# Performance work log

Measured on AMD Instinct MI355X. Metric: run time of the kernel, lower is better.

## Reference

```python
import jax, jax.numpy as jnp
import numpy as np

NUM_HEADS = 8
NUM_GROUPS = 32  # min(32, channels=256)
EPS = 1e-5


def group_norm(x, w, b):
    # x: [B, C, L]
    B, C, L = x.shape
    xg = x.reshape(B, NUM_GROUPS, C // NUM_GROUPS, L)
    mu = xg.mean(axis=(2, 3), keepdims=True)
    var = xg.var(axis=(2, 3), keepdims=True)
    xn = ((xg - mu) * jax.lax.rsqrt(var + EPS)).reshape(B, C, L)
    return xn * w[None, :, None] + b[None, :, None]


def setup_inputs() -> dict:
    key = jax.random.key(0)
    ks = jax.random.split(key, 5)
    B, C, L = 4, 256, 2048
    x = jax.random.normal(ks[0], (B, C, L), dtype=jnp.float32)
    gn_w = jnp.ones((C,), dtype=jnp.float32)
    gn_b = jnp.zeros((C,), dtype=jnp.float32)
    qkv_w = jax.random.normal(ks[1], (3 * C, C), dtype=jnp.float32) * (C ** -0.5)
    qkv_b = jax.random.normal(ks[2], (3 * C,), dtype=jnp.float32) * 0.02
    out_w = jax.random.normal(ks[3], (C, C), dtype=jnp.float32) * (C ** -0.5)
    out_b = jax.random.normal(ks[4], (C,), dtype=jnp.float32) * 0.02
    return {"x": x, "gn_w": gn_w, "gn_b": gn_b, "qkv_w": qkv_w,
            "qkv_b": qkv_b, "out_w": out_w, "out_b": out_b}


def reference(x, gn_w, gn_b, qkv_w, qkv_b, out_w, out_b):
    B, C, L = x.shape
    H = NUM_HEADS
    D = C // H
    h = group_norm(x, gn_w, gn_b)
    # 1x1 conv == channel matmul: [B,3C,L]
    qkv = jnp.einsum('oc,bcl->bol', qkv_w, h) + qkv_b[None, :, None]
    qkv = qkv.reshape(B, 3, H, D, L)
    q, k, v = qkv[:, 0], qkv[:, 1], qkv[:, 2]  # each [B,H,D,L]
    scale = D ** -0.5
    attn = jnp.einsum('bhdn,bhdm->bhnm', q * scale, k)  # [B,H,L,L]
    attn = jax.nn.softmax(attn, axis=-1)
    h = jnp.einsum('bhnm,bhdm->bhdn', attn, v).reshape(B, C, L)
    out = jnp.einsum('oc,bcl->bol', out_w, h) + out_b[None, :, None]
    return x + out
```

## Files before the change

### kernel.cpp

```cpp
#include <hip/hip_runtime.h>
#include <math.h>

using f32x4  = __attribute__((ext_vector_type(4))) float;
using bf16x8 = __attribute__((ext_vector_type(8))) short;

constexpr int kB = 4, kC = 256, kL = 2048, kH = 8;
constexpr float kQScale = 0.25505402264f;

__device__ __forceinline__ unsigned short f2bf(float f) {
    unsigned u = __builtin_bit_cast(unsigned, f);
    u += 0x7fffu + ((u >> 16) & 1u);
    return (unsigned short)(u >> 16);
}
__device__ __forceinline__ unsigned cvt_pk(float lo, float hi) {
    unsigned r;
    asm("v_cvt_pk_bf16_f32 %0, %1, %2" : "=v"(r) : "v"(lo), "v"(hi));
    return r;
}
__device__ __forceinline__ f32x4 mfma16(bf16x8 a, bf16x8 b, f32x4 c) {
    return __builtin_amdgcn_mfma_f32_16x16x32_bf16(a, b, c, 0, 0, 0);
}
__device__ __forceinline__ bf16x8 bc8(unsigned a, unsigned b, unsigned c, unsigned d) {
    return __builtin_bit_cast(bf16x8, make_uint4(a, b, c, d));
}
__device__ __forceinline__ void glds16(const unsigned short* g, unsigned short* l) {
    __builtin_amdgcn_global_load_lds(
        (const __attribute__((address_space(1))) unsigned int*)g,
        (__attribute__((address_space(3))) unsigned int*)l, 16, 0, 0);
}

__global__ __launch_bounds__(256) void gncvt_kernel(const float* __restrict__ x,
                                                    const float* __restrict__ gw,
                                                    const float* __restrict__ gb,
                                                    unsigned short* __restrict__ hT,
                                                    const float* __restrict__ qkvw,
                                                    const float* __restrict__ outw,
                                                    unsigned short* __restrict__ wq,
                                                    unsigned short* __restrict__ wo) {
    if (blockIdx.x >= 128) {
        int i = (blockIdx.x - 128) * 256 + threadIdx.x;
        const float* s; unsigned short* d; int j;
        if (i < 49152) { s = qkvw; d = wq; j = i; }
        else           { s = outw; d = wo; j = i - 49152; }
        float4 v = ((const float4*)s)[j];
        ((uint2*)d)[j] = make_uint2(cvt_pk(v.x, v.y), cvt_pk(v.z, v.w));
        return;
    }
    int b = blockIdx.x >> 5, g = blockIdx.x & 31;
    int t = threadIdx.x;
    const float* xp = x + ((size_t)b * kC + g * 8) * kL + 8 * t;

    float v[8][8];
    float s = 0.f, ss = 0.f;
#pragma unroll
    for (int c = 0; c < 8; ++c) {
        float4 a  = *(const float4*)(xp + (size_t)c * kL);
        float4 a2 = *(const float4*)(xp + (size_t)c * kL + 4);
        v[c][0]=a.x; v[c][1]=a.y; v[c][2]=a.z; v[c][3]=a.w;
        v[c][4]=a2.x; v[c][5]=a2.y; v[c][6]=a2.z; v[c][7]=a2.w;
        s  += (a.x+a.y)+(a.z+a.w)+(a2.x+a2.y)+(a2.z+a2.w);
        ss += a.x*a.x+a.y*a.y+a.z*a.z+a.w*a.w+a2.x*a2.x+a2.y*a2.y+a2.z*a2.z+a2.w*a2.w;
    }
#pragma unroll
    for (int off = 32; off; off >>= 1) {
        s  += __shfl_down(s, off);
        ss += __shfl_down(ss, off);
    }
    __shared__ float red[8];
    int wv = t >> 6;
    if ((t & 63) == 0) { red[wv] = s; red[4 + wv] = ss; }
    __syncthreads();
    s  = red[0] + red[1] + red[2] + red[3];
    ss = red[4] + red[5] + red[6] + red[7];
    float mean = s * (1.f / 16384.f);
    float var  = ss * (1.f / 16384.f) - mean * mean;
    float rstd = rsqrtf(var + 1e-5f);

    float wc[8], bc[8];
#pragma unroll
    for (int c = 0; c < 8; ++c) { wc[c] = gw[g*8+c] * rstd; bc[c] = gb[g*8+c]; }

    unsigned short* hp = hT + ((size_t)b * kL + 8 * t) * kC + g * 8;
#pragma unroll
    for (int j = 0; j < 8; ++j) {
        unsigned pk[4];
#pragma unroll
        for (int c2 = 0; c2 < 4; ++c2) {
            pk[c2] = cvt_pk((v[2*c2  ][j] - mean) * wc[2*c2  ] + bc[2*c2  ],
                            (v[2*c2+1][j] - mean) * wc[2*c2+1] + bc[2*c2+1]);
        }
        *(uint4*)(hp + (size_t)j * kC) = make_uint4(pk[0], pk[1], pk[2], pk[3]);
    }
}

__device__ __forceinline__ void store_qk(unsigned short* __restrict__ base, size_t bh,
                                         int n, int d0, f32x4 acc,
                                         const float* bias4, float scale) {
    float v0 = (acc[0] + bias4[0]) * scale, v1 = (acc[1] + bias4[1]) * scale;
    float v2 = (acc[2] + bias4[2]) * scale, v3 = (acc[3] + bias4[3]) * scale;
    *(uint2*)(base + (bh * kL + n) * 32 + d0) = make_uint2(cvt_pk(v0, v1), cvt_pk(v2, v3));
}

__global__ __launch_bounds__(256) void qkv_gemm(const unsigned short* __restrict__ Wb,
                                                const unsigned short* __restrict__ hT,
                                                const float* __restrict__ qkvb,
                                                unsigned short* __restrict__ qT,
                                                unsigned short* __restrict__ kT,
                                                unsigned short* __restrict__ vbuf) {
    __shared__ alignas(16) unsigned short Hlds[2][8][512];
    int t = threadIdx.x, wv = t >> 6, ll = t & 15, lg = (t >> 4) & 3;
    int lane = t & 63;
    int n0 = blockIdx.x * 128, o0 = blockIdx.y * 64, b = blockIdx.z;
    int obase = o0 + wv * 16;
    const unsigned short* hb = hT + (size_t)b * kL * kC;

    bf16x8 wf[8];
#pragma unroll
    for (int k = 0; k < 8; ++k)
        wf[k] = *(const bf16x8*)(Wb + (size_t)(obase + ll) * 256 + 32 * k + 8 * lg);
    float bias[4];
#pragma unroll
    for (int r = 0; r < 4; ++r) bias[r] = qkvb[obase + 4 * lg + r];
    int mode = (obase < 256) ? 0 : (obase < 512 ? 1 : 2);
    int d0 = (obase & 31) + 4 * lg;

    const unsigned short* hsrc0 = hb + (size_t)(n0 + 16 * (2 * wv)     + ll) * 256 + 8 * lg;
    const unsigned short* hsrc1 = hb + (size_t)(n0 + 16 * (2 * wv + 1) + ll) * 256 + 8 * lg;

    glds16(hsrc0,      &Hlds[0][2 * wv][0]);
    glds16(hsrc1,      &Hlds[0][2 * wv + 1][0]);
    glds16(hsrc0 + 32, &Hlds[1][2 * wv][0]);
    glds16(hsrc1 + 32, &Hlds[1][2 * wv + 1][0]);
    asm volatile("s_waitcnt vmcnt(2)" ::: "memory");
    __builtin_amdgcn_sched_barrier(0);
    __builtin_amdgcn_s_barrier();

    f32x4 acc[8] = {};
    int cur = 0;
    for (int c = 0; c < 8; ++c) {
        bf16x8 hf[8];
#pragma unroll
        for (int nj = 0; nj < 8; ++nj)
            hf[nj] = *(const bf16x8*)&Hlds[cur][nj][lane * 8];
        asm volatile("s_waitcnt lgkmcnt(0)" ::: "memory");
        __builtin_amdgcn_sched_barrier(0);
        __builtin_amdgcn_s_barrier();

        int kn = ((c + 2) & 7) * 32;
        glds16(hsrc0 + kn, &Hlds[cur][2 * wv][0]);
        glds16(hsrc1 + kn, &Hlds[cur][2 * wv + 1][0]);

        __builtin_amdgcn_s_setprio(1);
#pragma unroll
        for (int nj = 0; nj < 8; ++nj)
            acc[nj] = mfma16(wf[c], hf[nj], acc[nj]);
        __builtin_amdgcn_s_setprio(0);

        asm volatile("s_waitcnt vmcnt(2)" ::: "memory");
        __builtin_amdgcn_sched_barrier(0);
        __builtin_amdgcn_s_barrier();
        cur ^= 1;
    }
    asm volatile("s_waitcnt vmcnt(0)" ::: "memory");

#pragma unroll
    for (int nj = 0; nj < 8; ++nj) {
        int n = n0 + 16 * nj + ll;
        if (mode == 0) {
            store_qk(qT, (size_t)b * kH + (obase >> 5), n, d0, acc[nj], bias, kQScale);
        } else if (mode == 1) {
            store_qk(kT, (size_t)b * kH + ((obase - 256) >> 5), n, d0, acc[nj], bias, 1.f);
        } else {
#pragma unroll
            for (int r = 0; r < 4; ++r) {
                size_t row = (size_t)b * kC + (obase - 512) + 4 * lg + r;
                vbuf[row * kL + n] = f2bf(acc[nj][r] + bias[r]);
            }
        }
    }
}

__global__ __launch_bounds__(256) void attn_kernel(const unsigned short* __restrict__ qT,
                                                   const unsigned short* __restrict__ kT,
                                                   const unsigned short* __restrict__ vbuf,
                                                   unsigned short* __restrict__ h2T) {
    __shared__ alignas(16) unsigned short Klds[2][4][512];
    __shared__ alignas(16) unsigned short Vlds[2][4][512];
    __shared__ unsigned Plds[4][16][34];
    int t = threadIdx.x, wv = t >> 6, ll = t & 15, hi = (t >> 4) & 3;
    int lane = t & 63;
    int j = blockIdx.x;
    int bid = (j & 7) * 128 + (j >> 3);
    int qg = bid & 31, bh = bid >> 5;
    int b = bh >> 3, h = bh & 7;
    const unsigned short* qb = qT + (size_t)bh * kL * 32;
    const unsigned short* kb = kT + (size_t)bh * kL * 32;
    const unsigned short* vb = vbuf + ((size_t)b * kC + h * 32) * kL;
    int nq = qg * 64 + wv * 16;

    bf16x8 qf = *(const bf16x8*)(qb + (size_t)(nq + ll) * 32 + 8 * hi);

    f32x4 acc[2] = {};
    float lsum = 0.f;
    const f32x4 zero = {0.f, 0.f, 0.f, 0.f};

    const unsigned short* ksrc = kb + (size_t)(16 * wv + ll) * 32 + 8 * hi;
    const unsigned short* vsrc = vb + (size_t)(16 * (wv >> 1) + ll) * kL + 32 * (wv & 1) + 8 * hi;

    glds16(ksrc, &Klds[0][wv][0]);
    glds16(vsrc, &Vlds[0][wv][0]);
    glds16(ksrc + (size_t)64 * 32, &Klds[1][wv][0]);
    glds16(vsrc + 64,              &Vlds[1][wv][0]);
    asm volatile("s_waitcnt vmcnt(2)" ::: "memory");
    __builtin_amdgcn_sched_barrier(0);
    __builtin_amdgcn_s_barrier();

    int cur = 0;
    for (int it = 0; it < 32; ++it) {
        bf16x8 ka[4], va[2][2];
#pragma unroll
        for (int mj = 0; mj < 4; ++mj)
            ka[mj] = *(const bf16x8*)&Klds[cur][mj][lane * 8];
#pragma unroll
        for (int dj = 0; dj < 2; ++dj)
#pragma unroll
            for (int tt = 0; tt < 2; ++tt)
                va[dj][tt] = *(const bf16x8*)&Vlds[cur][dj * 2 + tt][lane * 8];

        asm volatile("s_waitcnt lgkmcnt(0)" ::: "memory");
        __builtin_amdgcn_sched_barrier(0);
        __builtin_amdgcn_s_barrier();

        int kn = ((it + 2) & 31) * 64;
        glds16(ksrc + (size_t)kn * 32, &Klds[cur][wv][0]);
        glds16(vsrc + kn,              &Vlds[cur][wv][0]);

        f32x4 s[4];
        __builtin_amdgcn_s_setprio(1);
#pragma unroll
        for (int mj = 0; mj < 4; ++mj)
            s[mj] = mfma16(ka[mj], qf, zero);
        __builtin_amdgcn_s_setprio(0);

#pragma unroll
        for (int mj = 0; mj < 4; ++mj) {
            float p0 = __builtin_amdgcn_exp2f(s[mj][0]);
            float p1 = __builtin_amdgcn_exp2f(s[mj][1]);
            float p2 = __builtin_amdgcn_exp2f(s[mj][2]);
            float p3 = __builtin_amdgcn_exp2f(s[mj][3]);
            lsum += (p0 + p1) + (p2 + p3);
            *(uint2*)&Plds[wv][ll][8 * mj + 2 * hi] =
                make_uint2(cvt_pk(p0, p1), cvt_pk(p2, p3));
        }

        bf16x8 pbf[2];
#pragma unroll
        for (int tt = 0; tt < 2; ++tt) {
            uint2 lo  = *(uint2*)&Plds[wv][ll][16 * tt + 4 * hi];
            uint2 hi2 = *(uint2*)&Plds[wv][ll][16 * tt + 4 * hi + 2];
            pbf[tt] = bc8(lo.x, lo.y, hi2.x, hi2.y);
        }

        __builtin_amdgcn_s_setprio(1);
#pragma unroll
        for (int tt = 0; tt < 2; ++tt)
#pragma unroll
            for (int dj = 0; dj < 2; ++dj)
                acc[dj] = mfma16(va[dj][tt], pbf[tt], acc[dj]);
        __builtin_amdgcn_s_setprio(0);

        asm volatile("s_waitcnt vmcnt(2)" ::: "memory");
        __builtin_amdgcn_sched_barrier(0);
        __builtin_amdgcn_s_barrier();
        cur ^= 1;
    }
    asm volatile("s_waitcnt vmcnt(0)" ::: "memory");

    lsum += __shfl_xor(lsum, 16);
    lsum += __shfl_xor(lsum, 32);
    float inv = 1.f / lsum;
    unsigned short* ob = h2T + ((size_t)b * kL + nq + ll) * kC + h * 32;
    *(uint2*)(ob + 4 * hi)      = make_uint2(cvt_pk(acc[0][0] * inv, acc[0][1] * inv),
                                             cvt_pk(acc[0][2] * inv, acc[0][3] * inv));
    *(uint2*)(ob + 16 + 4 * hi) = make_uint2(cvt_pk(acc[1][0] * inv, acc[1][1] * inv),
                                             cvt_pk(acc[1][2] * inv, acc[1][3] * inv));
}

__global__ __launch_bounds__(256) void out_gemm(const unsigned short* __restrict__ Wb,
                                                const unsigned short* __restrict__ h2T,
                                                const float* __restrict__ outb,
                                                const float* __restrict__ x,
                                                float* __restrict__ out) {
    __shared__ alignas(16) unsigned short Hlds[2][4][512];
    int t = threadIdx.x, wv = t >> 6, ll = t & 15, lg = (t >> 4) & 3;
    int lane = t & 63;
    int n0 = blockIdx.x * 64, o0 = blockIdx.y * 64, b = blockIdx.z;
    int obase = o0 + wv * 16;
    const unsigned short* hb = h2T + (size_t)b * kL * kC;

    bf16x8 wf[8];
#pragma unroll
    for (int k = 0; k < 8; ++k)
        wf[k] = *(const bf16x8*)(Wb + (size_t)(obase + ll) * 256 + 32 * k + 8 * lg);
    float bias[4];
#pragma unroll
    for (int r = 0; r < 4; ++r) bias[r] = outb[obase + 4 * lg + r];

    const unsigned short* hsrc = hb + (size_t)(n0 + 16 * wv + ll) * 256 + 8 * lg;

    glds16(hsrc,      &Hlds[0][wv][0]);
    glds16(hsrc + 32, &Hlds[1][wv][0]);
    asm volatile("s_waitcnt vmcnt(1)" ::: "memory");
    __builtin_amdgcn_sched_barrier(0);
    __builtin_amdgcn_s_barrier();

    f32x4 acc[4] = {};
    int cur = 0;
    for (int c = 0; c < 8; ++c) {
        bf16x8 hf[4];
#pragma unroll
        for (int nj = 0; nj < 4; ++nj)
            hf[nj] = *(const bf16x8*)&Hlds[cur][nj][lane * 8];
        asm volatile("s_waitcnt lgkmcnt(0)" ::: "memory");
        __builtin_amdgcn_sched_barrier(0);
        __builtin_amdgcn_s_barrier();

        int kn = ((c + 2) & 7) * 32;
        glds16(hsrc + kn, &Hlds[cur][wv][0]);

        __builtin_amdgcn_s_setprio(1);
#pragma unroll
        for (int nj = 0; nj < 4; ++nj)
            acc[nj] = mfma16(wf[c], hf[nj], acc[nj]);
        __builtin_amdgcn_s_setprio(0);

        asm volatile("s_waitcnt vmcnt(1)" ::: "memory");
        __builtin_amdgcn_sched_barrier(0);
        __builtin_amdgcn_s_barrier();
        cur ^= 1;
    }
    asm volatile("s_waitcnt vmcnt(0)" ::: "memory");

#pragma unroll
    for (int nj = 0; nj < 4; ++nj) {
        int n = n0 + 16 * nj + ll;
#pragma unroll
        for (int r = 0; r < 4; ++r) {
            size_t row = (size_t)b * kC + obase + 4 * lg + r;
            out[row * kL + n] = acc[nj][r] + bias[r] + x[row * kL + n];
        }
    }
}

extern "C" void kernel_launch(void* const* d_in, const int* in_sizes, int n_in,
                              void* d_out, int out_size, void* d_ws, size_t ws_size,
                              hipStream_t stream) {
    const float* x     = (const float*)d_in[0];
    const float* gn_w  = (const float*)d_in[1];
    const float* gn_b  = (const float*)d_in[2];
    const float* qkv_w = (const float*)d_in[3];
    const float* qkv_b = (const float*)d_in[4];
    const float* out_w = (const float*)d_in[5];
    const float* out_b = (const float*)d_in[6];
    float* out = (float*)d_out;

    char* ws = (char*)d_ws;
    const size_t MB = 1024 * 1024;
    unsigned short* hT   = (unsigned short*)(ws);
    unsigned short* qT   = (unsigned short*)(ws + 4  * MB);
    unsigned short* kT   = (unsigned short*)(ws + 8  * MB);
    unsigned short* vbuf = (unsigned short*)(ws + 12 * MB);
    unsigned short* h2T  = (unsigned short*)(ws + 16 * MB);
    unsigned short* wqkv = (unsigned short*)(ws + 20 * MB);
    unsigned short* wout = (unsigned short*)(ws + 20 * MB + 512 * 1024);

    gncvt_kernel<<<dim3(384), 256, 0, stream>>>(x, gn_w, gn_b, hT, qkv_w, out_w, wqkv, wout);
    qkv_gemm<<<dim3(16, 12, kB), 256, 0, stream>>>(wqkv, hT, qkv_b, qT, kT, vbuf);
    attn_kernel<<<dim3(1024), 256, 0, stream>>>(qT, kT, vbuf, h2T);
    out_gemm<<<dim3(32, 4, kB), 256, 0, stream>>>(wout, h2T, out_b, x, out);
}
```

Before: 71.01 us.

## Drop LDS staging of P and V by permuting key order in PV MFMA

Reorders the key index inside each 32-key chunk so each lane's packed bf16 probabilities from the QK^T MFMA output serve directly as the B operand of the PV MFMA. This removes the per-iteration round-trip of P through shared memory. V is now read straight from global memory with 8-byte loads in the matching permuted order, replacing the double-buffered LDS prefetch of V. This saves shared-memory traffic and LDS footprint. In exchange, the V loads are no longer prefetched ahead of use, so their global/L2 latency may be exposed each iteration, and the loads are narrower and strided.

```diff
diff --git a/kernel.cpp b/kernel.cpp
--- a/kernel.cpp
+++ b/kernel.cpp
@@ -185,8 +185,6 @@
                                                    const unsigned short* __restrict__ vbuf,
                                                    unsigned short* __restrict__ h2T) {
     __shared__ alignas(16) unsigned short Klds[2][4][512];
-    __shared__ alignas(16) unsigned short Vlds[2][4][512];
-    __shared__ unsigned Plds[4][16][34];
     int t = threadIdx.x, wv = t >> 6, ll = t & 15, hi = (t >> 4) & 3;
     int lane = t & 63;
     int j = blockIdx.x;
@@ -205,27 +203,30 @@
     const f32x4 zero = {0.f, 0.f, 0.f, 0.f};
 
     const unsigned short* ksrc = kb + (size_t)(16 * wv + ll) * 32 + 8 * hi;
-    const unsigned short* vsrc = vb + (size_t)(16 * (wv >> 1) + ll) * kL + 32 * (wv & 1) + 8 * hi;
+    const int vo0 = ll * kL + 4 * hi;
+    const int vo1 = (16 + ll) * kL + 4 * hi;
 
     glds16(ksrc, &Klds[0][wv][0]);
-    glds16(vsrc, &Vlds[0][wv][0]);
     glds16(ksrc + (size_t)64 * 32, &Klds[1][wv][0]);
-    glds16(vsrc + 64,              &Vlds[1][wv][0]);
-    asm volatile("s_waitcnt vmcnt(2)" ::: "memory");
+    asm volatile("s_waitcnt vmcnt(1)" ::: "memory");
     __builtin_amdgcn_sched_barrier(0);
     __builtin_amdgcn_s_barrier();
 
     int cur = 0;
     for (int it = 0; it < 32; ++it) {
-        bf16x8 ka[4], va[2][2];
+        int m0 = it * 64;
+        bf16x8 ka[4];
 #pragma unroll
         for (int mj = 0; mj < 4; ++mj)
             ka[mj] = *(const bf16x8*)&Klds[cur][mj][lane * 8];
-#pragma unroll
-        for (int dj = 0; dj < 2; ++dj)
-#pragma unroll
-            for (int tt = 0; tt < 2; ++tt)
-                va[dj][tt] = *(const bf16x8*)&Vlds[cur][dj * 2 + tt][lane * 8];
+        uint2 va[2][2][2];
+#pragma unroll
+        for (int u = 0; u < 2; ++u)
+#pragma unroll
+            for (int hf = 0; hf < 2; ++hf) {
+                va[0][u][hf] = *(const uint2*)(vb + vo0 + m0 + 32 * u + 16 * hf);
+                va[1][u][hf] = *(const uint2*)(vb + vo1 + m0 + 32 * u + 16 * hf);
+            }
 
         asm volatile("s_waitcnt lgkmcnt(0)" ::: "memory");
         __builtin_amdgcn_sched_barrier(0);
@@ -233,7 +234,6 @@
 
         int kn = ((it + 2) & 31) * 64;
         glds16(ksrc + (size_t)kn * 32, &Klds[cur][wv][0]);
-        glds16(vsrc + kn,              &Vlds[cur][wv][0]);
 
         f32x4 s[4];
         __builtin_amdgcn_s_setprio(1);
@@ -242,6 +242,7 @@
             s[mj] = mfma16(ka[mj], qf, zero);
         __builtin_amdgcn_s_setprio(0);
 
+        unsigned w[4][2];
 #pragma unroll
         for (int mj = 0; mj < 4; ++mj) {
             float p0 = __builtin_amdgcn_exp2f(s[mj][0]);
@@ -249,27 +250,22 @@
             float p2 = __builtin_amdgcn_exp2f(s[mj][2]);
             float p3 = __builtin_amdgcn_exp2f(s[mj][3]);
             lsum += (p0 + p1) + (p2 + p3);
-            *(uint2*)&Plds[wv][ll][8 * mj + 2 * hi] =
-                make_uint2(cvt_pk(p0, p1), cvt_pk(p2, p3));
-        }
-
-        bf16x8 pbf[2];
-#pragma unroll
-        for (int tt = 0; tt < 2; ++tt) {
-            uint2 lo  = *(uint2*)&Plds[wv][ll][16 * tt + 4 * hi];
-            uint2 hi2 = *(uint2*)&Plds[wv][ll][16 * tt + 4 * hi + 2];
-            pbf[tt] = bc8(lo.x, lo.y, hi2.x, hi2.y);
+            w[mj][0] = cvt_pk(p0, p1);
+            w[mj][1] = cvt_pk(p2, p3);
         }
 
         __builtin_amdgcn_s_setprio(1);
 #pragma unroll
-        for (int tt = 0; tt < 2; ++tt)
-#pragma unroll
-            for (int dj = 0; dj < 2; ++dj)
-                acc[dj] = mfma16(va[dj][tt], pbf[tt], acc[dj]);
+        for (int u = 0; u < 2; ++u) {
+            bf16x8 pb  = bc8(w[2*u][0], w[2*u][1], w[2*u+1][0], w[2*u+1][1]);
+            bf16x8 va0 = bc8(va[0][u][0].x, va[0][u][0].y, va[0][u][1].x, va[0][u][1].y);
+            bf16x8 va1 = bc8(va[1][u][0].x, va[1][u][0].y, va[1][u][1].x, va[1][u][1].y);
+            acc[0] = mfma16(va0, pb, acc[0]);
+            acc[1] = mfma16(va1, pb, acc[1]);
+        }
         __builtin_amdgcn_s_setprio(0);
 
-        asm volatile("s_waitcnt vmcnt(2)" ::: "memory");
+        asm volatile("s_waitcnt vmcnt(1)" ::: "memory");
         __builtin_amdgcn_sched_barrier(0);
         __builtin_amdgcn_s_barrier();
         cur ^= 1;
```

After: 161.0 us. 127% more time.
